# Kernel optimization log

Hardware: AMD Instinct MI355X
Metric: run time of the kernel (lower is better)

Reference implementation:

```python
import jax, jax.numpy as jnp
import numpy as np

TEMPERATURE = 0.07
BASE_TEMPERATURE = 0.07
ANCHOR_NUM = 256   # total_classes after hard-anchor sampling
N_VIEW = 16
FEAT_DIM = 256
NUM_CLASSES = 19


def setup_inputs() -> dict:
    key = jax.random.key(0)
    k1, k2 = jax.random.split(key)
    feats = jax.random.normal(k1, (ANCHOR_NUM, N_VIEW, FEAT_DIM), dtype=jnp.float32)
    # projection-head outputs are L2-normalized in the upstream network
    feats = feats / jnp.linalg.norm(feats, axis=-1, keepdims=True)
    labels = jax.random.randint(k2, (ANCHOR_NUM,), 0, NUM_CLASSES, dtype=jnp.int32)
    return {"feats": feats, "labels": labels}


def reference(feats, labels) -> jnp.ndarray:
    # feats: [A, V, D] sampled anchors; labels: [A] class ids
    A, V, D = feats.shape
    N = A * V
    dt = feats.dtype
    # torch.cat(torch.unbind(feats_, dim=1), dim=0) -> view-major ordering
    contrast = feats.transpose(1, 0, 2).reshape(N, D)          # [N, D]
    lbl = jnp.tile(labels, V)                                   # [N]

    logits = jnp.matmul(contrast, contrast.T) / jnp.asarray(TEMPERATURE, dt)  # [N, N]
    logits = logits - jax.lax.stop_gradient(jnp.max(logits, axis=1, keepdims=True))

    pos_mask = (lbl[:, None] == lbl[None, :]).astype(dt)        # [N, N]
    neg_mask = 1.0 - pos_mask
    diag = jnp.arange(N)
    pos_mask = pos_mask.at[diag, diag].set(0.0)                 # drop self-contrast

    exp_logits = jnp.exp(logits)
    neg_sum = jnp.sum(exp_logits * neg_mask, axis=1, keepdims=True)  # [N, 1]
    log_prob = logits - jnp.log(exp_logits + neg_sum)
    mean_log_prob_pos = jnp.sum(pos_mask * log_prob, axis=1) / jnp.sum(pos_mask, axis=1)
    loss = -(TEMPERATURE / BASE_TEMPERATURE) * mean_log_prob_pos
    return jnp.mean(loss)
```

## Files before the change

### kernel.cpp

```cpp
#include <hip/hip_runtime.h>
#include <hip/hip_bf16.h>

#define D_DIM   256
#define N_TOT   4096
#define N_ANCH  256
#define NCOLG   32
#define NPART   64
#define K1  20.60992915555662f
#define LN2 0.6931471805599453f
#define MAXNP    48

typedef __attribute__((ext_vector_type(8))) short bf16x8;
typedef __attribute__((ext_vector_type(4))) float f32x4;

#define MFMA(a, b, c) __builtin_amdgcn_mfma_f32_16x16x32_bf16((a), (b), (c), 0, 0, 0)

__device__ __forceinline__ ushort f2bf(float f) {
    union { float f; unsigned u; } a; a.f = f;
    unsigned u = a.u;
    u = (u + 0x7FFFu + ((u >> 16) & 1u)) >> 16;
    return (ushort)u;
}

__global__ void __launch_bounds__(256) k_convert(const float* __restrict__ feats,
                                                 const int* __restrict__ labels,
                                                 ushort* __restrict__ xb,
                                                 int* __restrict__ cntW,
                                                 int* __restrict__ posRank,
                                                 int* __restrict__ tileOff) {
    int idx = blockIdx.x * 256 + threadIdx.x;
    int base = idx * 4;
    float4 v = *(const float4*)(feats + base);
    ushort4 o;
    o.x = f2bf(v.x); o.y = f2bf(v.y); o.z = f2bf(v.z); o.w = f2bf(v.w);
    *(ushort4*)(xb + base) = o;

    if (blockIdx.x == 0) {
        __shared__ int labS[N_ANCH];
        __shared__ int cntS[32];
        int t = threadIdx.x;
        if (t < 32) cntS[t] = 0;
        labS[t] = labels[t];
        __syncthreads();
        atomicAdd(&cntS[labS[t]], 1);
        __syncthreads();
        int myLab = labS[t];
        int rank = 0, toff = 0;
        for (int b = 0; b < t; ++b) {
            int lb = labS[b];
            rank += (lb == myLab);
            toff += cntS[lb];
        }
        posRank[t] = rank;
        tileOff[t] = toff;
        if (t < 32) cntW[t] = cntS[t];
    }
}

__global__ void __launch_bounds__(256, 2) k_pass1(const ushort* __restrict__ xb,
                                                  const int* __restrict__ labels,
                                                  const int* __restrict__ posRank,
                                                  const int* __restrict__ tileOff,
                                                  float* __restrict__ partAll,
                                                  float* __restrict__ posBuf) {
    __shared__ __align__(16) char lds[65536];

    const int g = blockIdx.x >> 5;
    const int s = blockIdx.x & 31;
    const int tid = threadIdx.x;
    const int lane = tid & 63, wid = tid >> 6;
    const int lrow = lane & 15, khalf = lane >> 4;
    const int wr = wid >> 1, wc = wid & 1;

    const char* aSrc = (const char*)(xb + (size_t)g * 128 * D_DIM);
    const char* bSrc = (const char*)(xb + (size_t)s * 128 * D_DIM);

    uint32_t Lg[8], Lw[8];
#pragma unroll
    for (int o = 0; o < 8; ++o) {
        uint32_t L = (uint32_t)(tid * 16 + o * 4096);
        Lg[o] = (L >> 8) * 512 + (L & 255);
        Lw[o] = L ^ (((L >> 8) & 7u) << 4);
    }

    bf16x8 stA[8], stB[8];
    auto loadch = [&](int kc) {
#pragma unroll
        for (int o = 0; o < 8; ++o) {
            stA[o] = *(const bf16x8*)(aSrc + Lg[o] + kc * 256);
            stB[o] = *(const bf16x8*)(bSrc + Lg[o] + kc * 256);
        }
    };
    auto writelds = [&]() {
#pragma unroll
        for (int o = 0; o < 8; ++o) {
            *(bf16x8*)(lds + Lw[o])         = stA[o];
            *(bf16x8*)(lds + 32768 + Lw[o]) = stB[o];
        }
    };

    f32x4 acc[4][4];
#pragma unroll
    for (int m = 0; m < 4; ++m)
#pragma unroll
        for (int n = 0; n < 4; ++n)
            acc[m][n] = (f32x4){0.f, 0.f, 0.f, 0.f};

    const uint32_t swz = (uint32_t)((lrow & 7) << 4);
    auto compute = [&]() {
#pragma unroll
        for (int ks = 0; ks < 4; ++ks) {
            bf16x8 af[4], bfr[4];
#pragma unroll
            for (int m = 0; m < 4; ++m) {
                uint32_t row = (uint32_t)(wr * 64 + m * 16 + lrow);
                af[m] = *(const bf16x8*)(lds + ((row * 256 + ks * 64 + khalf * 16) ^ swz));
            }
#pragma unroll
            for (int n = 0; n < 4; ++n) {
                uint32_t row = (uint32_t)(wc * 64 + n * 16 + lrow);
                bfr[n] = *(const bf16x8*)(lds + 32768 + ((row * 256 + ks * 64 + khalf * 16) ^ swz));
            }
#pragma unroll
            for (int m = 0; m < 4; ++m)
#pragma unroll
                for (int n = 0; n < 4; ++n)
                    acc[m][n] = MFMA(af[m], bfr[n], acc[m][n]);
        }
    };

    loadch(0);
    writelds();
    __syncthreads();
    loadch(1);
    compute();
    __syncthreads();
    writelds();
    __syncthreads();
    compute();

    const int raBase = g * 8 + wr * 4, caBase = s * 8 + wc * 4;
    int labR[4], offR[4], labC[4], rankC[4];
#pragma unroll
    for (int m = 0; m < 4; ++m) {
        labR[m] = labels[raBase + m];
        offR[m] = tileOff[raBase + m];
    }
#pragma unroll
    for (int n = 0; n < 4; ++n) {
        labC[n] = labels[caBase + n];
        rankC[n] = posRank[caBase + n];
    }

    float aAll[4][4];
#pragma unroll
    for (int m = 0; m < 4; ++m)
#pragma unroll
        for (int i = 0; i < 4; ++i) aAll[m][i] = 0.f;

#pragma unroll
    for (int m = 0; m < 4; ++m) {
#pragma unroll
        for (int n = 0; n < 4; ++n) {
            f32x4 c = acc[m][n];
#pragma unroll
            for (int i = 0; i < 4; ++i)
                aAll[m][i] += exp2f(__builtin_fmaf(c[i], K1, -K1));
            if (labR[m] == labC[n])
                *(f32x4*)(posBuf + (size_t)(offR[m] + rankC[n]) * 256 + lane * 4) = c;
        }
    }

#pragma unroll
    for (int msk = 1; msk < 16; msk <<= 1)
#pragma unroll
        for (int m = 0; m < 4; ++m)
#pragma unroll
            for (int i = 0; i < 4; ++i)
                aAll[m][i] += __shfl_xor(aAll[m][i], msk, 64);

    if (lrow == 0) {
#pragma unroll
        for (int m = 0; m < 4; ++m)
#pragma unroll
            for (int i = 0; i < 4; ++i) {
                int row = g * 128 + wr * 64 + m * 16 + khalf * 4 + i;
                partAll[row * NPART + s * 2 + wc] = aAll[m][i];
            }
    }
}

__global__ void __launch_bounds__(256) k_passB(const float* __restrict__ posBuf,
                                               const int* __restrict__ labels,
                                               const int* __restrict__ cntW,
                                               const int* __restrict__ posRank,
                                               const int* __restrict__ tileOff,
                                               const float* __restrict__ partAll,
                                               float* __restrict__ partOut) {
    int rt  = blockIdx.x;
    int tid = threadIdx.x;
    int l = tid >> 2, i = tid & 3;
    int r   = (l >> 4) * 4 + i;
    int col = l & 15;

    int np       = cntW[labels[rt]];
    int off      = tileOff[rt];
    int selfRank = posRank[rt];

    __shared__ float tile[MAXNP * 256];
    __shared__ float shA[16][17];
    __shared__ float shB[16][17];
    __shared__ float nsSh[16], PSh[16];

    float sE = 0.f, sP = 0.f;
    const float* src = posBuf + (size_t)off * 256 + tid;
    for (int j = 0; j < np; ++j) {
        float c = src[j * 256];
        tile[j * 256 + tid] = c;
        float l2 = __builtin_fmaf(c, K1, -K1);
        sE += exp2f(l2);
        bool diag = (j == selfRank) & (col == r);
        sP += diag ? 0.f : l2;
    }
    shA[r][col] = sE;
    shB[r][col] = sP;
    __syncthreads();
    if (tid < 16) {
        float e = 0.f, p = 0.f;
#pragma unroll
        for (int cc = 0; cc < 16; ++cc) { e += shA[tid][cc]; p += shB[tid][cc]; }
        const float* pa = partAll + (rt * 16 + tid) * NPART;
        float sall = 0.f;
#pragma unroll
        for (int q = 0; q < 16; ++q) {
            float4 v = *(const float4*)(pa + q * 4);
            sall += v.x + v.y + v.z + v.w;
        }
        nsSh[tid] = sall - e;
        PSh[tid]  = p;
    }
    __syncthreads();

    float nsv = nsSh[r];
    float sL = 0.f;
    for (int j = 0; j < np; ++j) {
        float c  = tile[j * 256 + tid];
        float l2 = __builtin_fmaf(c, K1, -K1);
        float lg = __log2f(exp2f(l2) + nsv);
        bool diag = (j == selfRank) & (col == r);
        sL += diag ? 0.f : lg;
    }
    __syncthreads();
    shA[r][col] = sL;
    __syncthreads();
    if (tid < 16) {
        float L = 0.f;
#pragma unroll
        for (int cc = 0; cc < 16; ++cc) L += shA[tid][cc];
        float npRow = (float)(16 * np - 1);
        shB[0][tid] = (PSh[tid] - L) / npRow;
    }
    __syncthreads();
    if (tid == 0) {
        float sx = 0.f;
#pragma unroll
        for (int q = 0; q < 16; ++q) sx += shB[0][q];
        partOut[rt] = sx;
    }
}

__global__ void __launch_bounds__(256) k_final(const float* __restrict__ partOut,
                                               float* __restrict__ out) {
    __shared__ float red[256];
    int t = threadIdx.x;
    red[t] = partOut[t];
    __syncthreads();
    for (int o = 128; o; o >>= 1) {
        if (t < o) red[t] += red[t + o];
        __syncthreads();
    }
    if (t == 0) out[0] = -red[0] * (LN2 / (float)N_TOT);
}

extern "C" void kernel_launch(void* const* d_in, const int* in_sizes, int n_in,
                              void* d_out, int out_size, void* d_ws, size_t ws_size,
                              hipStream_t stream) {
    const float* feats  = (const float*)d_in[0];
    const int*   labels = (const int*)d_in[1];
    float* out = (float*)d_out;

    char* ws = (char*)d_ws;
    ushort* xb      = (ushort*)ws;
    float*  partAll = (float*)(ws + (2u << 20));
    float*  posBuf  = (float*)(ws + (3u << 20));
    char*   meta    = ws + (11u << 20);
    int*    cntW    = (int*)meta;
    int*    posRank = (int*)(meta + 128);
    int*    tileOff = (int*)(meta + 128 + 1024);
    float*  partOut = (float*)(meta + 128 + 2048);

    k_convert<<<1024, 256, 0, stream>>>(feats, labels, xb, cntW, posRank, tileOff);
    k_pass1  <<<1024, 256, 0, stream>>>(xb, labels, posRank, tileOff, partAll, posBuf);
    k_passB  <<<N_ANCH, 256, 0, stream>>>(posBuf, labels, cntW, posRank, tileOff, partAll, partOut);
    k_final  <<<1, 256, 0, stream>>>(partOut, out);
}
```

Measured before the change: 37.09 us.

## Fuse per-anchor loss and final reduction into GEMM kernel via completion counters

```diff
diff --git a/kernel.cpp b/kernel.cpp
--- a/kernel.cpp
+++ b/kernel.cpp
@@ -4,7 +4,6 @@
 #define D_DIM   256
 #define N_TOT   4096
 #define N_ANCH  256
-#define NCOLG   32
 #define NPART   64
 #define K1  20.60992915555662f
 #define LN2 0.6931471805599453f
@@ -22,12 +21,13 @@
     return (ushort)u;
 }
 
-__global__ void __launch_bounds__(256) k_convert(const float* __restrict__ feats,
-                                                 const int* __restrict__ labels,
-                                                 ushort* __restrict__ xb,
-                                                 int* __restrict__ cntW,
-                                                 int* __restrict__ posRank,
-                                                 int* __restrict__ tileOff) {
+__global__ void __launch_bounds__(256) k_prep(const float* __restrict__ feats,
+                                              const int* __restrict__ labels,
+                                              ushort* __restrict__ xb,
+                                              int* __restrict__ cntW,
+                                              int* __restrict__ posRank,
+                                              int* __restrict__ tileOff,
+                                              int* __restrict__ ctrs) {
     int idx = blockIdx.x * 256 + threadIdx.x;
     int base = idx * 4;
     float4 v = *(const float4*)(feats + base);
@@ -39,6 +39,7 @@
         __shared__ int labS[N_ANCH];
         __shared__ int cntS[32];
         int t = threadIdx.x;
+        if (t < 33) ctrs[t] = 0;
         if (t < 32) cntS[t] = 0;
         labS[t] = labels[t];
         __syncthreads();
@@ -57,13 +58,21 @@
     }
 }
 
-__global__ void __launch_bounds__(256, 2) k_pass1(const ushort* __restrict__ xb,
-                                                  const int* __restrict__ labels,
-                                                  const int* __restrict__ posRank,
-                                                  const int* __restrict__ tileOff,
-                                                  float* __restrict__ partAll,
-                                                  float* __restrict__ posBuf) {
+__global__ void __launch_bounds__(256, 2) k_mega(const ushort* __restrict__ xb,
+                                                 const int* __restrict__ labels,
+                                                 const int* __restrict__ posRank,
+                                                 const int* __restrict__ tileOff,
+                                                 const int* __restrict__ cntW,
+                                                 float* __restrict__ partAll,
+                                                 float* __restrict__ posBuf,
+                                                 float* __restrict__ partOut,
+                                                 int* __restrict__ ctrs,
+                                                 float* __restrict__ out) {
     __shared__ __align__(16) char lds[65536];
+    __shared__ float shA[16][17];
+    __shared__ float shB[16][17];
+    __shared__ float nsSh[16], PSh[16];
+    __shared__ int winS;
 
     const int g = blockIdx.x >> 5;
     const int s = blockIdx.x & 31;
@@ -72,214 +81,221 @@
     const int lrow = lane & 15, khalf = lane >> 4;
     const int wr = wid >> 1, wc = wid & 1;
 
-    const char* aSrc = (const char*)(xb + (size_t)g * 128 * D_DIM);
-    const char* bSrc = (const char*)(xb + (size_t)s * 128 * D_DIM);
-
-    uint32_t Lg[8], Lw[8];
-#pragma unroll
-    for (int o = 0; o < 8; ++o) {
-        uint32_t L = (uint32_t)(tid * 16 + o * 4096);
-        Lg[o] = (L >> 8) * 512 + (L & 255);
-        Lw[o] = L ^ (((L >> 8) & 7u) << 4);
-    }
-
-    bf16x8 stA[8], stB[8];
-    auto loadch = [&](int kc) {
+    {
+        const char* aSrc = (const char*)(xb + (size_t)g * 128 * D_DIM);
+        const char* bSrc = (const char*)(xb + (size_t)s * 128 * D_DIM);
+
+        uint32_t Lg[8], Lw[8];
 #pragma unroll
         for (int o = 0; o < 8; ++o) {
-            stA[o] = *(const bf16x8*)(aSrc + Lg[o] + kc * 256);
-            stB[o] = *(const bf16x8*)(bSrc + Lg[o] + kc * 256);
-        }
-    };
-    auto writelds = [&]() {
-#pragma unroll
-        for (int o = 0; o < 8; ++o) {
-            *(bf16x8*)(lds + Lw[o])         = stA[o];
-            *(bf16x8*)(lds + 32768 + Lw[o]) = stB[o];
-        }
-    };
-
-    f32x4 acc[4][4];
-#pragma unroll
-    for (int m = 0; m < 4; ++m)
-#pragma unroll
-        for (int n = 0; n < 4; ++n)
-            acc[m][n] = (f32x4){0.f, 0.f, 0.f, 0.f};
-
-    const uint32_t swz = (uint32_t)((lrow & 7) << 4);
-    auto compute = [&]() {
-#pragma unroll
-        for (int ks = 0; ks < 4; ++ks) {
-            bf16x8 af[4], bfr[4];
-#pragma unroll
-            for (int m = 0; m < 4; ++m) {
-                uint32_t row = (uint32_t)(wr * 64 + m * 16 + lrow);
-                af[m] = *(const bf16x8*)(lds + ((row * 256 + ks * 64 + khalf * 16) ^ swz));
-            }
+            uint32_t L = (uint32_t)(tid * 16 + o * 4096);
+            Lg[o] = (L >> 8) * 512 + (L & 255);
+            Lw[o] = L ^ (((L >> 8) & 7u) << 4);
+        }
+
+        bf16x8 stA[8], stB[8];
+        auto loadch = [&](int kc) {
+#pragma unroll
+            for (int o = 0; o < 8; ++o) {
+                stA[o] = *(const bf16x8*)(aSrc + Lg[o] + kc * 256);
+                stB[o] = *(const bf16x8*)(bSrc + Lg[o] + kc * 256);
+            }
+        };
+        auto writelds = [&]() {
+#pragma unroll
+            for (int o = 0; o < 8; ++o) {
+                *(bf16x8*)(lds + Lw[o])         = stA[o];
+                *(bf16x8*)(lds + 32768 + Lw[o]) = stB[o];
+            }
+        };
+
+        f32x4 acc[4][4];
+#pragma unroll
+        for (int m = 0; m < 4; ++m)
+#pragma unroll
+            for (int n = 0; n < 4; ++n)
+                acc[m][n] = (f32x4){0.f, 0.f, 0.f, 0.f};
+
+        const uint32_t swz = (uint32_t)((lrow & 7) << 4);
+        auto compute = [&]() {
+#pragma unroll
+            for (int ks = 0; ks < 4; ++ks) {
+                bf16x8 af[4], bfr[4];
+#pragma unroll
+                for (int m = 0; m < 4; ++m) {
+                    uint32_t row = (uint32_t)(wr * 64 + m * 16 + lrow);
+                    af[m] = *(const bf16x8*)(lds + ((row * 256 + ks * 64 + khalf * 16) ^ swz));
+                }
+#pragma unroll
+                for (int n = 0; n < 4; ++n) {
+                    uint32_t row = (uint32_t)(wc * 64 + n * 16 + lrow);
+                    bfr[n] = *(const bf16x8*)(lds + 32768 + ((row * 256 + ks * 64 + khalf * 16) ^ swz));
+                }
+#pragma unroll
+                for (int m = 0; m < 4; ++m)
+#pragma unroll
+                    for (int n = 0; n < 4; ++n)
+                        acc[m][n] = MFMA(af[m], bfr[n], acc[m][n]);
+            }
+        };
+
+        loadch(0);
+        writelds();
+        __syncthreads();
+        loadch(1);
+        compute();
+        __syncthreads();
+        writelds();
+        __syncthreads();
+        compute();
+
+        const int raBase = g * 8 + wr * 4, caBase = s * 8 + wc * 4;
+        int labR[4], offR[4], labC[4], rankC[4];
+#pragma unroll
+        for (int m = 0; m < 4; ++m) {
+            labR[m] = labels[raBase + m];
+            offR[m] = tileOff[raBase + m];
+        }
+#pragma unroll
+        for (int n = 0; n < 4; ++n) {
+            labC[n] = labels[caBase + n];
+            rankC[n] = posRank[caBase + n];
+        }
+
+        float aAll[4][4];
+#pragma unroll
+        for (int m = 0; m < 4; ++m)
+#pragma unroll
+            for (int i = 0; i < 4; ++i) aAll[m][i] = 0.f;
+
+#pragma unroll
+        for (int m = 0; m < 4; ++m) {
 #pragma unroll
             for (int n = 0; n < 4; ++n) {
-                uint32_t row = (uint32_t)(wc * 64 + n * 16 + lrow);
-                bfr[n] = *(const bf16x8*)(lds + 32768 + ((row * 256 + ks * 64 + khalf * 16) ^ swz));
-            }
+                f32x4 c = acc[m][n];
+#pragma unroll
+                for (int i = 0; i < 4; ++i)
+                    aAll[m][i] += exp2f(__builtin_fmaf(c[i], K1, -K1));
+                if (labR[m] == labC[n])
+                    *(f32x4*)(posBuf + (size_t)(offR[m] + rankC[n]) * 256 + lane * 4) = c;
+            }
+        }
+
+#pragma unroll
+        for (int msk = 1; msk < 16; msk <<= 1)
 #pragma unroll
             for (int m = 0; m < 4; ++m)
 #pragma unroll
-                for (int n = 0; n < 4; ++n)
-                    acc[m][n] = MFMA(af[m], bfr[n], acc[m][n]);
-        }
-    };
-
-    loadch(0);
-    writelds();
-    __syncthreads();
-    loadch(1);
-    compute();
-    __syncthreads();
-    writelds();
-    __syncthreads();
-    compute();
-
-    const int raBase = g * 8 + wr * 4, caBase = s * 8 + wc * 4;
-    int labR[4], offR[4], labC[4], rankC[4];
-#pragma unroll
-    for (int m = 0; m < 4; ++m) {
-        labR[m] = labels[raBase + m];
-        offR[m] = tileOff[raBase + m];
-    }
-#pragma unroll
-    for (int n = 0; n < 4; ++n) {
-        labC[n] = labels[caBase + n];
-        rankC[n] = posRank[caBase + n];
-    }
-
-    float aAll[4][4];
-#pragma unroll
-    for (int m = 0; m < 4; ++m)
-#pragma unroll
-        for (int i = 0; i < 4; ++i) aAll[m][i] = 0.f;
-
-#pragma unroll
-    for (int m = 0; m < 4; ++m) {
-#pragma unroll
-        for (int n = 0; n < 4; ++n) {
-            f32x4 c = acc[m][n];
-#pragma unroll
-            for (int i = 0; i < 4; ++i)
-                aAll[m][i] += exp2f(__builtin_fmaf(c[i], K1, -K1));
-            if (labR[m] == labC[n])
-                *(f32x4*)(posBuf + (size_t)(offR[m] + rankC[n]) * 256 + lane * 4) = c;
-        }
-    }
-
-#pragma unroll
-    for (int msk = 1; msk < 16; msk <<= 1)
-#pragma unroll
-        for (int m = 0; m < 4; ++m)
-#pragma unroll
-            for (int i = 0; i < 4; ++i)
-                aAll[m][i] += __shfl_xor(aAll[m][i], msk, 64);
-
-    if (lrow == 0) {
-#pragma unroll
-        for (int m = 0; m < 4; ++m)
-#pragma unroll
-            for (int i = 0; i < 4; ++i) {
-                int row = g * 128 + wr * 64 + m * 16 + khalf * 4 + i;
-                partAll[row * NPART + s * 2 + wc] = aAll[m][i];
-            }
-    }
-}
-
-__global__ void __launch_bounds__(256) k_passB(const float* __restrict__ posBuf,
-                                               const int* __restrict__ labels,
-                                               const int* __restrict__ cntW,
-                                               const int* __restrict__ posRank,
-                                               const int* __restrict__ tileOff,
-                                               const float* __restrict__ partAll,
-                                               float* __restrict__ partOut) {
-    int rt  = blockIdx.x;
-    int tid = threadIdx.x;
-    int l = tid >> 2, i = tid & 3;
-    int r   = (l >> 4) * 4 + i;
-    int col = l & 15;
-
-    int np       = cntW[labels[rt]];
-    int off      = tileOff[rt];
-    int selfRank = posRank[rt];
-
-    __shared__ float tile[MAXNP * 256];
-    __shared__ float shA[16][17];
-    __shared__ float shB[16][17];
-    __shared__ float nsSh[16], PSh[16];
-
-    float sE = 0.f, sP = 0.f;
-    const float* src = posBuf + (size_t)off * 256 + tid;
-    for (int j = 0; j < np; ++j) {
-        float c = src[j * 256];
-        tile[j * 256 + tid] = c;
-        float l2 = __builtin_fmaf(c, K1, -K1);
-        sE += exp2f(l2);
-        bool diag = (j == selfRank) & (col == r);
-        sP += diag ? 0.f : l2;
-    }
-    shA[r][col] = sE;
-    shB[r][col] = sP;
-    __syncthreads();
-    if (tid < 16) {
-        float e = 0.f, p = 0.f;
-#pragma unroll
-        for (int cc = 0; cc < 16; ++cc) { e += shA[tid][cc]; p += shB[tid][cc]; }
-        const float* pa = partAll + (rt * 16 + tid) * NPART;
-        float sall = 0.f;
-#pragma unroll
-        for (int q = 0; q < 16; ++q) {
-            float4 v = *(const float4*)(pa + q * 4);
-            sall += v.x + v.y + v.z + v.w;
-        }
-        nsSh[tid] = sall - e;
-        PSh[tid]  = p;
-    }
-    __syncthreads();
-
-    float nsv = nsSh[r];
-    float sL = 0.f;
-    for (int j = 0; j < np; ++j) {
-        float c  = tile[j * 256 + tid];
-        float l2 = __builtin_fmaf(c, K1, -K1);
-        float lg = __log2f(exp2f(l2) + nsv);
-        bool diag = (j == selfRank) & (col == r);
-        sL += diag ? 0.f : lg;
-    }
-    __syncthreads();
-    shA[r][col] = sL;
-    __syncthreads();
-    if (tid < 16) {
-        float L = 0.f;
-#pragma unroll
-        for (int cc = 0; cc < 16; ++cc) L += shA[tid][cc];
-        float npRow = (float)(16 * np - 1);
-        shB[0][tid] = (PSh[tid] - L) / npRow;
-    }
+                for (int i = 0; i < 4; ++i)
+                    aAll[m][i] += __shfl_xor(aAll[m][i], msk, 64);
+
+        if (lrow == 0) {
+#pragma unroll
+            for (int m = 0; m < 4; ++m)
+#pragma unroll
+                for (int i = 0; i < 4; ++i) {
+                    int row = g * 128 + wr * 64 + m * 16 + khalf * 4 + i;
+                    partAll[row * NPART + s * 2 + wc] = aAll[m][i];
+                }
+        }
+    }
+
     __syncthreads();
     if (tid == 0) {
-        float sx = 0.f;
-#pragma unroll
-        for (int q = 0; q < 16; ++q) sx += shB[0][q];
-        partOut[rt] = sx;
-    }
-}
-
-__global__ void __launch_bounds__(256) k_final(const float* __restrict__ partOut,
-                                               float* __restrict__ out) {
-    __shared__ float red[256];
-    int t = threadIdx.x;
-    red[t] = partOut[t];
-    __syncthreads();
-    for (int o = 128; o; o >>= 1) {
-        if (t < o) red[t] += red[t + o];
-        __syncthreads();
-    }
-    if (t == 0) out[0] = -red[0] * (LN2 / (float)N_TOT);
+        __threadfence();
+        winS = (atomicAdd(&ctrs[g], 1) == 31);
+    }
+    __syncthreads();
+    if (!winS) return;
+    __threadfence();
+
+    float* tile = (float*)lds;
+    const int l = tid >> 2, ii = tid & 3;
+    const int r   = (l >> 4) * 4 + ii;
+    const int col = l & 15;
+    float myAcc = 0.f;
+
+    for (int aIdx = 0; aIdx < 8; ++aIdx) {
+        int rt = g * 8 + aIdx;
+        int np       = cntW[labels[rt]];
+        int off      = tileOff[rt];
+        int selfRank = posRank[rt];
+        __syncthreads();
+
+        float sE = 0.f, sP = 0.f;
+        const float* src = posBuf + (size_t)off * 256 + tid;
+        for (int j = 0; j < np; ++j) {
+            float c = src[j * 256];
+            tile[j * 256 + tid] = c;
+            float l2 = __builtin_fmaf(c, K1, -K1);
+            sE += exp2f(l2);
+            bool diag = (j == selfRank) & (col == r);
+            sP += diag ? 0.f : l2;
+        }
+        shA[r][col] = sE;
+        shB[r][col] = sP;
+        __syncthreads();
+        if (tid < 16) {
+            float e = 0.f, p = 0.f;
+#pragma unroll
+            for (int cc = 0; cc < 16; ++cc) { e += shA[tid][cc]; p += shB[tid][cc]; }
+            const float* pa = partAll + (size_t)(rt * 16 + tid) * NPART;
+            float sall = 0.f;
+#pragma unroll
+            for (int q = 0; q < 16; ++q) {
+                float4 v = *(const float4*)(pa + q * 4);
+                sall += v.x + v.y + v.z + v.w;
+            }
+            nsSh[tid] = sall - e;
+            PSh[tid]  = p;
+        }
+        __syncthreads();
+
+        float nsv = nsSh[r];
+        float sL = 0.f;
+        for (int j = 0; j < np; ++j) {
+            float c  = tile[j * 256 + tid];
+            float l2 = __builtin_fmaf(c, K1, -K1);
+            float lg = __log2f(exp2f(l2) + nsv);
+            bool diag = (j == selfRank) & (col == r);
+            sL += diag ? 0.f : lg;
+        }
+        __syncthreads();
+        shA[r][col] = sL;
+        __syncthreads();
+        if (tid < 16) {
+            float L = 0.f;
+#pragma unroll
+            for (int cc = 0; cc < 16; ++cc) L += shA[tid][cc];
+            myAcc += (PSh[tid] - L) / (float)(16 * np - 1);
+        }
+    }
+
+    __syncthreads();
+    if (tid < 16) shA[0][tid] = myAcc;
+    __syncthreads();
+    if (tid == 0) {
+        float gs = 0.f;
+#pragma unroll
+        for (int q = 0; q < 16; ++q) gs += shA[0][q];
+        partOut[g] = gs;
+    }
+
+    __syncthreads();
+    if (tid == 0) {
+        __threadfence();
+        winS = (atomicAdd(&ctrs[32], 1) == 31);
+    }
+    __syncthreads();
+    if (!winS) return;
+    __threadfence();
+
+    if (tid < 64) {
+        float v = (tid < 32) ? partOut[tid] : 0.f;
+#pragma unroll
+        for (int m = 1; m <= 16; m <<= 1) v += __shfl_xor(v, m, 64);
+        if (tid == 0) out[0] = -v * (LN2 / (float)N_TOT);
+    }
 }
 
 extern "C" void kernel_launch(void* const* d_in, const int* in_sizes, int n_in,
@@ -298,9 +314,9 @@
     int*    posRank = (int*)(meta + 128);
     int*    tileOff = (int*)(meta + 128 + 1024);
     float*  partOut = (float*)(meta + 128 + 2048);
-
-    k_convert<<<1024, 256, 0, stream>>>(feats, labels, xb, cntW, posRank, tileOff);
-    k_pass1  <<<1024, 256, 0, stream>>>(xb, labels, posRank, tileOff, partAll, posBuf);
-    k_passB  <<<N_ANCH, 256, 0, stream>>>(posBuf, labels, cntW, posRank, tileOff, partAll, partOut);
-    k_final  <<<1, 256, 0, stream>>>(partOut, out);
+    int*    ctrs    = (int*)(meta + 128 + 2048 + 256);
+
+    k_prep<<<1024, 256, 0, stream>>>(feats, labels, xb, cntW, posRank, tileOff, ctrs);
+    k_mega<<<1024, 256, 0, stream>>>(xb, labels, posRank, tileOff, cntW,
+                                     partAll, posBuf, partOut, ctrs, out);
 }
```

New measurement: 120.7 us. +225.5%, slower.

## Halve GEMM LDS tile for higher occupancy and fold final reduction into passB

Applied to the files above, without the earlier changes.

```diff
diff --git a/kernel.cpp b/kernel.cpp
--- a/kernel.cpp
+++ b/kernel.cpp
@@ -4,7 +4,6 @@
 #define D_DIM   256
 #define N_TOT   4096
 #define N_ANCH  256
-#define NCOLG   32
 #define NPART   64
 #define K1  20.60992915555662f
 #define LN2 0.6931471805599453f
@@ -22,12 +21,13 @@
     return (ushort)u;
 }
 
-__global__ void __launch_bounds__(256) k_convert(const float* __restrict__ feats,
-                                                 const int* __restrict__ labels,
-                                                 ushort* __restrict__ xb,
-                                                 int* __restrict__ cntW,
-                                                 int* __restrict__ posRank,
-                                                 int* __restrict__ tileOff) {
+__global__ void __launch_bounds__(256) k_prep(const float* __restrict__ feats,
+                                              const int* __restrict__ labels,
+                                              ushort* __restrict__ xb,
+                                              int* __restrict__ cntW,
+                                              int* __restrict__ posRank,
+                                              int* __restrict__ tileOff,
+                                              int* __restrict__ ctrs) {
     int idx = blockIdx.x * 256 + threadIdx.x;
     int base = idx * 4;
     float4 v = *(const float4*)(feats + base);
@@ -39,6 +39,7 @@
         __shared__ int labS[N_ANCH];
         __shared__ int cntS[32];
         int t = threadIdx.x;
+        if (t < 4) ctrs[t] = 0;
         if (t < 32) cntS[t] = 0;
         labS[t] = labels[t];
         __syncthreads();
@@ -57,13 +58,13 @@
     }
 }
 
-__global__ void __launch_bounds__(256, 2) k_pass1(const ushort* __restrict__ xb,
+__global__ void __launch_bounds__(256, 3) k_pass1(const ushort* __restrict__ xb,
                                                   const int* __restrict__ labels,
                                                   const int* __restrict__ posRank,
                                                   const int* __restrict__ tileOff,
                                                   float* __restrict__ partAll,
                                                   float* __restrict__ posBuf) {
-    __shared__ __align__(16) char lds[65536];
+    __shared__ __align__(16) char lds[32768];
 
     const int g = blockIdx.x >> 5;
     const int s = blockIdx.x & 31;
@@ -75,27 +76,27 @@
     const char* aSrc = (const char*)(xb + (size_t)g * 128 * D_DIM);
     const char* bSrc = (const char*)(xb + (size_t)s * 128 * D_DIM);
 
-    uint32_t Lg[8], Lw[8];
-#pragma unroll
-    for (int o = 0; o < 8; ++o) {
+    uint32_t Lg[4], Lw[4];
+#pragma unroll
+    for (int o = 0; o < 4; ++o) {
         uint32_t L = (uint32_t)(tid * 16 + o * 4096);
-        Lg[o] = (L >> 8) * 512 + (L & 255);
-        Lw[o] = L ^ (((L >> 8) & 7u) << 4);
-    }
-
-    bf16x8 stA[8], stB[8];
+        Lg[o] = (L >> 7) * 512 + (L & 127);
+        Lw[o] = L ^ (((L >> 7) & 7u) << 4);
+    }
+
+    bf16x8 stA[4], stB[4];
     auto loadch = [&](int kc) {
 #pragma unroll
-        for (int o = 0; o < 8; ++o) {
-            stA[o] = *(const bf16x8*)(aSrc + Lg[o] + kc * 256);
-            stB[o] = *(const bf16x8*)(bSrc + Lg[o] + kc * 256);
+        for (int o = 0; o < 4; ++o) {
+            stA[o] = *(const bf16x8*)(aSrc + Lg[o] + kc * 128);
+            stB[o] = *(const bf16x8*)(bSrc + Lg[o] + kc * 128);
         }
     };
     auto writelds = [&]() {
 #pragma unroll
-        for (int o = 0; o < 8; ++o) {
+        for (int o = 0; o < 4; ++o) {
             *(bf16x8*)(lds + Lw[o])         = stA[o];
-            *(bf16x8*)(lds + 32768 + Lw[o]) = stB[o];
+            *(bf16x8*)(lds + 16384 + Lw[o]) = stB[o];
         }
     };
 
@@ -109,17 +110,17 @@
     const uint32_t swz = (uint32_t)((lrow & 7) << 4);
     auto compute = [&]() {
 #pragma unroll
-        for (int ks = 0; ks < 4; ++ks) {
+        for (int ks = 0; ks < 2; ++ks) {
             bf16x8 af[4], bfr[4];
 #pragma unroll
             for (int m = 0; m < 4; ++m) {
                 uint32_t row = (uint32_t)(wr * 64 + m * 16 + lrow);
-                af[m] = *(const bf16x8*)(lds + ((row * 256 + ks * 64 + khalf * 16) ^ swz));
+                af[m] = *(const bf16x8*)(lds + ((row * 128 + ks * 64 + khalf * 16) ^ swz));
             }
 #pragma unroll
             for (int n = 0; n < 4; ++n) {
                 uint32_t row = (uint32_t)(wc * 64 + n * 16 + lrow);
-                bfr[n] = *(const bf16x8*)(lds + 32768 + ((row * 256 + ks * 64 + khalf * 16) ^ swz));
+                bfr[n] = *(const bf16x8*)(lds + 16384 + ((row * 128 + ks * 64 + khalf * 16) ^ swz));
             }
 #pragma unroll
             for (int m = 0; m < 4; ++m)
@@ -132,12 +133,15 @@
     loadch(0);
     writelds();
     __syncthreads();
-    loadch(1);
-    compute();
-    __syncthreads();
-    writelds();
-    __syncthreads();
-    compute();
+    for (int kc = 0; kc < 4; ++kc) {
+        if (kc < 3) loadch(kc + 1);
+        compute();
+        if (kc < 3) {
+            __syncthreads();
+            writelds();
+            __syncthreads();
+        }
+    }
 
     const int raBase = g * 8 + wr * 4, caBase = s * 8 + wc * 4;
     int labR[4], offR[4], labC[4], rankC[4];
@@ -196,7 +200,9 @@
                                                const int* __restrict__ posRank,
                                                const int* __restrict__ tileOff,
                                                const float* __restrict__ partAll,
-                                               float* __restrict__ partOut) {
+                                               float* __restrict__ partOut,
+                                               int* __restrict__ ctrs,
+                                               float* __restrict__ out) {
     int rt  = blockIdx.x;
     int tid = threadIdx.x;
     int l = tid >> 2, i = tid & 3;
@@ -211,6 +217,8 @@
     __shared__ float shA[16][17];
     __shared__ float shB[16][17];
     __shared__ float nsSh[16], PSh[16];
+    __shared__ int winS;
+    __shared__ float red[256];
 
     float sE = 0.f, sP = 0.f;
     const float* src = posBuf + (size_t)off * 256 + tid;
@@ -229,7 +237,7 @@
         float e = 0.f, p = 0.f;
 #pragma unroll
         for (int cc = 0; cc < 16; ++cc) { e += shA[tid][cc]; p += shB[tid][cc]; }
-        const float* pa = partAll + (rt * 16 + tid) * NPART;
+        const float* pa = partAll + (size_t)(rt * 16 + tid) * NPART;
         float sall = 0.f;
 #pragma unroll
         for (int q = 0; q < 16; ++q) {
@@ -267,19 +275,23 @@
         for (int q = 0; q < 16; ++q) sx += shB[0][q];
         partOut[rt] = sx;
     }
-}
-
-__global__ void __launch_bounds__(256) k_final(const float* __restrict__ partOut,
-                                               float* __restrict__ out) {
-    __shared__ float red[256];
-    int t = threadIdx.x;
-    red[t] = partOut[t];
-    __syncthreads();
-    for (int o = 128; o; o >>= 1) {
-        if (t < o) red[t] += red[t + o];
+
+    __syncthreads();
+    if (tid == 0) {
+        __threadfence();
+        winS = (atomicAdd(&ctrs[0], 1) == N_ANCH - 1);
+    }
+    __syncthreads();
+    if (!winS) return;
+    __threadfence();
+
+    red[tid] = partOut[tid];
+    __syncthreads();
+    for (int o2 = 128; o2; o2 >>= 1) {
+        if (tid < o2) red[tid] += red[tid + o2];
         __syncthreads();
     }
-    if (t == 0) out[0] = -red[0] * (LN2 / (float)N_TOT);
+    if (tid == 0) out[0] = -red[0] * (LN2 / (float)N_TOT);
 }
 
 extern "C" void kernel_launch(void* const* d_in, const int* in_sizes, int n_in,
@@ -298,9 +310,10 @@
     int*    posRank = (int*)(meta + 128);
     int*    tileOff = (int*)(meta + 128 + 1024);
     float*  partOut = (float*)(meta + 128 + 2048);
-
-    k_convert<<<1024, 256, 0, stream>>>(feats, labels, xb, cntW, posRank, tileOff);
-    k_pass1  <<<1024, 256, 0, stream>>>(xb, labels, posRank, tileOff, partAll, posBuf);
-    k_passB  <<<N_ANCH, 256, 0, stream>>>(posBuf, labels, cntW, posRank, tileOff, partAll, partOut);
-    k_final  <<<1, 256, 0, stream>>>(partOut, out);
-}
+    int*    ctrs    = (int*)(meta + 128 + 2048 + 1024);
+
+    k_prep <<<1024, 256, 0, stream>>>(feats, labels, xb, cntW, posRank, tileOff, ctrs);
+    k_pass1<<<1024, 256, 0, stream>>>(xb, labels, posRank, tileOff, partAll, posBuf);
+    k_passB<<<N_ANCH, 256, 0, stream>>>(posBuf, labels, cntW, posRank, tileOff,
+                                        partAll, partOut, ctrs, out);
+}
```

After: 40.63 us. +9.6%, slower.

## Exploit Gram matrix symmetry: compute only upper-triangular tile pairs in pass1

Applied to the files above, without the earlier changes.

```diff
diff --git a/kernel.cpp b/kernel.cpp
--- a/kernel.cpp
+++ b/kernel.cpp
@@ -4,7 +4,8 @@
 #define D_DIM   256
 #define N_TOT   4096
 #define N_ANCH  256
-#define NCOLG   32
+#define NGRP    32
+#define NBLK    528
 #define NPART   64
 #define K1  20.60992915555662f
 #define LN2 0.6931471805599453f
@@ -65,8 +66,10 @@
                                                   float* __restrict__ posBuf) {
     __shared__ __align__(16) char lds[65536];
 
-    const int g = blockIdx.x >> 5;
-    const int s = blockIdx.x & 31;
+    int rem = blockIdx.x, g = 0;
+    while (rem >= NGRP - g) { rem -= NGRP - g; ++g; }
+    const int s = g + rem;
+
     const int tid = threadIdx.x;
     const int lane = tid & 63, wid = tid >> 6;
     const int lrow = lane & 15, khalf = lane >> 4;
@@ -138,36 +141,58 @@
     writelds();
     __syncthreads();
     compute();
+    __syncthreads();
 
     const int raBase = g * 8 + wr * 4, caBase = s * 8 + wc * 4;
-    int labR[4], offR[4], labC[4], rankC[4];
+    int labR[4], offR[4], rankR[4], labC[4], rankC[4], offC[4];
 #pragma unroll
     for (int m = 0; m < 4; ++m) {
-        labR[m] = labels[raBase + m];
-        offR[m] = tileOff[raBase + m];
+        labR[m]  = labels[raBase + m];
+        offR[m]  = tileOff[raBase + m];
+        rankR[m] = posRank[raBase + m];
     }
 #pragma unroll
     for (int n = 0; n < 4; ++n) {
-        labC[n] = labels[caBase + n];
+        labC[n]  = labels[caBase + n];
         rankC[n] = posRank[caBase + n];
+        offC[n]  = tileOff[caBase + n];
     }
 
     float aAll[4][4];
+    float colP[4];
 #pragma unroll
     for (int m = 0; m < 4; ++m)
 #pragma unroll
         for (int i = 0; i < 4; ++i) aAll[m][i] = 0.f;
+#pragma unroll
+    for (int n = 0; n < 4; ++n) colP[n] = 0.f;
+
+    float* scr = (float*)lds + wid * 256;
 
 #pragma unroll
     for (int m = 0; m < 4; ++m) {
 #pragma unroll
         for (int n = 0; n < 4; ++n) {
             f32x4 c = acc[m][n];
-#pragma unroll
-            for (int i = 0; i < 4; ++i)
-                aAll[m][i] += exp2f(__builtin_fmaf(c[i], K1, -K1));
-            if (labR[m] == labC[n])
+            float e[4];
+#pragma unroll
+            for (int i = 0; i < 4; ++i) {
+                e[i] = exp2f(__builtin_fmaf(c[i], K1, -K1));
+                aAll[m][i] += e[i];
+            }
+            if (g != s)
+                colP[n] += e[0] + e[1] + e[2] + e[3];
+            if (labR[m] == labC[n]) {
                 *(f32x4*)(posBuf + (size_t)(offR[m] + rankC[n]) * 256 + lane * 4) = c;
+                if (g != s) {
+#pragma unroll
+                    for (int i = 0; i < 4; ++i)
+                        scr[(khalf * 4 + i) * 16 + lrow] = c[i];
+                    __builtin_amdgcn_s_waitcnt(0);
+                    f32x4 tr = *(f32x4*)(scr + lrow * 16 + khalf * 4);
+                    *(f32x4*)(posBuf + (size_t)(offC[n] + rankR[m]) * 256 + lane * 4) = tr;
+                }
+            }
         }
     }
 
@@ -187,6 +212,21 @@
                 int row = g * 128 + wr * 64 + m * 16 + khalf * 4 + i;
                 partAll[row * NPART + s * 2 + wc] = aAll[m][i];
             }
+    }
+
+    if (g != s) {
+#pragma unroll
+        for (int msk = 16; msk < 64; msk <<= 1)
+#pragma unroll
+            for (int n = 0; n < 4; ++n)
+                colP[n] += __shfl_xor(colP[n], msk, 64);
+        if (lane < 16) {
+#pragma unroll
+            for (int n = 0; n < 4; ++n) {
+                int row = s * 128 + wc * 64 + n * 16 + lane;
+                partAll[row * NPART + g * 2 + wr] = colP[n];
+            }
+        }
     }
 }
 
@@ -229,7 +269,7 @@
         float e = 0.f, p = 0.f;
 #pragma unroll
         for (int cc = 0; cc < 16; ++cc) { e += shA[tid][cc]; p += shB[tid][cc]; }
-        const float* pa = partAll + (rt * 16 + tid) * NPART;
+        const float* pa = partAll + (size_t)(rt * 16 + tid) * NPART;
         float sall = 0.f;
 #pragma unroll
         for (int q = 0; q < 16; ++q) {
@@ -300,7 +340,8 @@
     float*  partOut = (float*)(meta + 128 + 2048);
 
     k_convert<<<1024, 256, 0, stream>>>(feats, labels, xb, cntW, posRank, tileOff);
-    k_pass1  <<<1024, 256, 0, stream>>>(xb, labels, posRank, tileOff, partAll, posBuf);
-    k_passB  <<<N_ANCH, 256, 0, stream>>>(posBuf, labels, cntW, posRank, tileOff, partAll, partOut);
+    k_pass1  <<<NBLK, 256, 0, stream>>>(xb, labels, posRank, tileOff, partAll, posBuf);
+    k_passB  <<<N_ANCH, 256, 0, stream>>>(posBuf, labels, cntW, posRank, tileOff,
+                                          partAll, partOut);
     k_final  <<<1, 256, 0, stream>>>(partOut, out);
 }
```

Result: no change. 37.44 us (+0.9%).
